# Kernel tuning notes

Hardware: AMD Instinct MI355X
Metric: run time of the kernel (lower is better)

The kernel has to match this reference:

```python
import jax, jax.numpy as jnp
import numpy as np


def setup_inputs() -> dict:
    key = jax.random.key(0)
    k1, k2, k3, k4, k5 = jax.random.split(key, 5)
    B, D, U = 16384, 512, 512
    scale = 1.0 / np.sqrt(D + U)
    return {
        "inputs": jax.random.normal(k1, (B, D), dtype=jnp.float32),
        "h_prev": jax.random.normal(k2, (B, U), dtype=jnp.float32),
        "Wz": jax.random.normal(k3, (D + U, U), dtype=jnp.float32) * scale,
        "Wr": jax.random.normal(k4, (D + U, U), dtype=jnp.float32) * scale,
        "Wh": jax.random.normal(k5, (D + U, U), dtype=jnp.float32) * scale,
    }


def reference(inputs, h_prev, Wz, Wr, Wh):
    # x_h: [B, D+U]
    x_h = jnp.concatenate([inputs, h_prev], axis=-1)
    z = jax.nn.sigmoid(x_h @ Wz)                     # update gate [B, U]
    r = jax.nn.sigmoid(x_h @ Wr)                     # reset gate  [B, U]
    h_hat = jnp.tanh(jnp.concatenate([inputs, r * h_prev], axis=-1) @ Wh)
    new_h = z * h_prev + (1.0 - z) * h_hat
    return new_h
```

## Files before the change

kernel.cpp:

```cpp
#include <hip/hip_runtime.h>
#include <hip/hip_bf16.h>
#include <stdint.h>

typedef __attribute__((ext_vector_type(8))) short short8;
typedef __attribute__((ext_vector_type(4))) float f32x4;
typedef unsigned short u16;

#define AS1 __attribute__((address_space(1)))
#define AS3 __attribute__((address_space(3)))

__device__ __forceinline__ u16 f2b(float f) {
  union { float f; uint32_t u; } c; c.f = f;
  uint32_t u = c.u;
  return (u16)((u + 0x7fffu + ((u >> 16) & 1u)) >> 16);
}
__device__ __forceinline__ float b2f(u16 b) {
  union { uint32_t u; float f; } c; c.u = ((uint32_t)b) << 16;
  return c.f;
}

__global__ void cvt_bf16_kernel(const float* __restrict__ src,
                                u16* __restrict__ dst, int n4) {
  int i = blockIdx.x * blockDim.x + threadIdx.x;
  if (i >= n4) return;
  const float4 v = reinterpret_cast<const float4*>(src)[i];
  ushort4 o;
  o.x = f2b(v.x); o.y = f2b(v.y); o.z = f2b(v.z); o.w = f2b(v.w);
  reinterpret_cast<ushort4*>(dst)[i] = o;
}

__global__ void cvt_transpose_kernel(const float* __restrict__ w0,
                                     const float* __restrict__ w1,
                                     const float* __restrict__ w2,
                                     u16* __restrict__ d0,
                                     u16* __restrict__ d1,
                                     u16* __restrict__ d2,
                                     int K, int N) {
  const float* src = (blockIdx.y == 0) ? w0 : (blockIdx.y == 1 ? w1 : w2);
  u16* dst = (blockIdx.y == 0) ? d0 : (blockIdx.y == 1 ? d1 : d2);
  int idx = blockIdx.x * blockDim.x + threadIdx.x;
  if (idx >= K * N) return;
  int k = idx / N, n = idx - k * N;
  dst[(size_t)n * K + k] = f2b(src[idx]);
}

#define BAR() __builtin_amdgcn_s_barrier()
#define VMW(n) asm volatile("s_waitcnt vmcnt(" #n ")" ::: "memory")

__global__ __launch_bounds__(512, 1) void gemm_gates_kernel(
    const u16* __restrict__ xb, const u16* __restrict__ hb,
    const u16* __restrict__ wt,
    u16* __restrict__ o_z, u16* __restrict__ o_rh) {
  constexpr int NT = 16, NITER = 8;
  __shared__ u16 lds[65536];
  const char* ldsb = (const char*)lds;

  const int tid = threadIdx.x;
  const int lane = tid & 63;
  const int wid = tid >> 6;
  const int wm = wid >> 2, wn = wid & 3;
  const int wg = ((int)blockIdx.x & 7) * 32 + ((int)blockIdx.x >> 3);
  const int bn = wg & 3, bm = wg >> 2;

  const int srow8 = tid >> 3;
  const int swzb = ((tid & 7) ^ (srow8 & 7)) << 4;
  auto STAGE = [&](int t, int kind) {
    if (t >= NT) return;
    u16* dst = lds + (t & 1) * 32768 + kind * 8192 + wid * 512;
    if (kind < 2) {
      const char* src = ((t < 8) ? ((const char*)xb + (size_t)t * 128)
                                 : ((const char*)hb + (size_t)(t - 8) * 128)) +
                        (size_t)(bm * 256 + kind * 128 + srow8) * 1024 + swzb;
      __builtin_amdgcn_global_load_lds((const AS1 void*)src, (AS3 void*)dst, 16, 0, 0);
      __builtin_amdgcn_global_load_lds((const AS1 void*)(src + 65536), (AS3 void*)(dst + 4096), 16, 0, 0);
    } else {
      const char* src = (const char*)wt +
                        (size_t)(bn * 256 + (kind - 2) * 128 + srow8) * 2048 +
                        (size_t)t * 128 + swzb;
      __builtin_amdgcn_global_load_lds((const AS1 void*)src, (AS3 void*)dst, 16, 0, 0);
      __builtin_amdgcn_global_load_lds((const AS1 void*)(src + 131072), (AS3 void*)(dst + 4096), 16, 0, 0);
    }
  };

  const int rsel = lane & 15;
  const int kg = lane >> 4;
  const int sl0 = (kg ^ (rsel & 7)) << 4;
  const int sl1 = ((4 + kg) ^ (rsel & 7)) << 4;
  const int aoff0 = wm * 16384 + rsel * 128;
  const int boff0 = 32768 + wn * 8192 + rsel * 128;

  f32x4 acc[8][4] = {};
  short8 a[4][2], b[4][2];

  auto ldA = [&](int DB, int mfb) {
#pragma unroll
    for (int mi = 0; mi < 4; ++mi) {
      a[mi][0] = *(const short8*)(ldsb + DB + aoff0 + (mfb + mi) * 2048 + sl0);
      a[mi][1] = *(const short8*)(ldsb + DB + aoff0 + (mfb + mi) * 2048 + sl1);
    }
  };
  auto ldB = [&](int DB, int nfb) {
#pragma unroll
    for (int ni = 0; ni < 2; ++ni) {
      b[nfb + ni][0] = *(const short8*)(ldsb + DB + boff0 + (nfb + ni) * 2048 + sl0);
      b[nfb + ni][1] = *(const short8*)(ldsb + DB + boff0 + (nfb + ni) * 2048 + sl1);
    }
  };
  auto MM = [&](int mb, int nb) {
    __builtin_amdgcn_s_setprio(1);
#pragma unroll
    for (int ks = 0; ks < 2; ++ks)
#pragma unroll
      for (int mi = 0; mi < 4; ++mi)
#pragma unroll
        for (int ni = 0; ni < 2; ++ni)
          acc[mb + mi][nb + ni] = __builtin_amdgcn_mfma_f32_16x16x32_bf16(
              a[mi][ks], b[nb + ni][ks], acc[mb + mi][nb + ni], 0, 0, 0);
    __builtin_amdgcn_s_setprio(0);
  };

  STAGE(0, 2); STAGE(0, 3); STAGE(0, 0); STAGE(0, 1); STAGE(1, 2); STAGE(1, 3);
  VMW(4); BAR();

#pragma unroll 1
  for (int j = 0; j < NITER; ++j) {
    const int t1 = 2 * j + 1, t2 = 2 * j + 2, t3 = 2 * j + 3;
    ldA(0, 0); ldB(0, 0); STAGE(t1, 0);
    BAR(); MM(0, 0); BAR();
    ldB(0, 2); STAGE(t1, 1);
    BAR(); MM(0, 2); BAR();
    ldA(0, 4); STAGE(t2, 2);
    BAR(); MM(4, 2); BAR();
    STAGE(t2, 3);
    BAR(); MM(4, 0);
    if (j == NITER - 1) { VMW(0); } else { VMW(4); }
    BAR();
    ldA(65536, 0); ldB(65536, 0); STAGE(t2, 0);
    BAR(); MM(0, 0); BAR();
    ldB(65536, 2); STAGE(t2, 1);
    BAR(); MM(0, 2); BAR();
    ldA(65536, 4); STAGE(t3, 2);
    BAR(); MM(4, 2); BAR();
    STAGE(t3, 3);
    BAR(); MM(4, 0);
    if (j == NITER - 1) { VMW(0); } else { VMW(4); }
    BAR();
  }

  const int row0 = bm * 256 + wm * 128 + kg * 4;
  const int col0 = bn * 256 + wn * 64 + rsel;
  if (bn < 2) {
#pragma unroll
    for (int mf = 0; mf < 8; ++mf)
#pragma unroll
      for (int nf = 0; nf < 4; ++nf)
#pragma unroll
        for (int q = 0; q < 4; ++q) {
          const int row = row0 + mf * 16 + q;
          const int col = col0 + nf * 16;
          const float zf = 1.f / (1.f + __expf(-acc[mf][nf][q]));
          o_z[(size_t)row * 512 + col] = f2b(zf);
        }
  } else {
#pragma unroll
    for (int mf = 0; mf < 8; ++mf)
#pragma unroll
      for (int nf = 0; nf < 4; ++nf)
#pragma unroll
        for (int q = 0; q < 4; ++q) {
          const int row = row0 + mf * 16 + q;
          const int col = col0 + nf * 16 - 512;
          const size_t idx = (size_t)row * 512 + col;
          const float rf = 1.f / (1.f + __expf(-acc[mf][nf][q]));
          o_rh[idx] = f2b(rf * b2f(hb[idx]));
        }
  }
}

__global__ __launch_bounds__(512, 1) void gemm_cand_kernel(
    const u16* __restrict__ xb, const u16* __restrict__ rhb,
    const u16* __restrict__ wt, const u16* __restrict__ hb,
    const u16* __restrict__ zb_in, float* __restrict__ o_f) {
  constexpr int NT = 16;
  __shared__ u16 lds[73728];
  const char* ldsb = (const char*)lds;

  const int tid = threadIdx.x;
  const int lane = tid & 63;
  const int wid = tid >> 6;
  const int wm = wid >> 2, wn = wid & 3;
  const int wg = ((int)blockIdx.x & 7) * 32 + ((int)blockIdx.x >> 3);
  const int bn = wg & 3, bm = wg >> 2;

  const int srow8 = tid >> 3;
  const int swzb = ((tid & 7) ^ (srow8 & 7)) << 4;
  auto STG_A = [&](int t, int half, int regionByte) {
    if (t >= NT) return;
    u16* dst = lds + regionByte / 2 + half * 8192 + wid * 512;
    const char* src = ((t < 8) ? ((const char*)xb + (size_t)t * 128)
                               : ((const char*)rhb + (size_t)(t - 8) * 128)) +
                      (size_t)(bm * 256 + half * 128 + srow8) * 1024 + swzb;
    __builtin_amdgcn_global_load_lds((const AS1 void*)src, (AS3 void*)dst, 16, 0, 0);
    __builtin_amdgcn_global_load_lds((const AS1 void*)(src + 65536), (AS3 void*)(dst + 4096), 16, 0, 0);
  };
  auto STG_B = [&](int t, int regionByte) {
    if (t >= NT) return;
    u16* dst = lds + regionByte / 2 + wid * 512;
    const char* src = (const char*)wt + (size_t)(bn * 128 + srow8) * 2048 +
                      (size_t)t * 128 + swzb;
    __builtin_amdgcn_global_load_lds((const AS1 void*)src, (AS3 void*)dst, 16, 0, 0);
    __builtin_amdgcn_global_load_lds((const AS1 void*)(src + 131072), (AS3 void*)(dst + 4096), 16, 0, 0);
  };

  const int rsel = lane & 15;
  const int kg = lane >> 4;
  const int sl0 = (kg ^ (rsel & 7)) << 4;
  const int sl1 = ((4 + kg) ^ (rsel & 7)) << 4;
  const int aoff0 = wm * 16384 + rsel * 128;
  const int boff0 = wn * 4096 + rsel * 128;

  f32x4 acc[8][2] = {};
  short8 a[4][2], b[2][2];

  auto RD_A = [&](int regionByte, int mfb) {
#pragma unroll
    for (int mi = 0; mi < 4; ++mi) {
      a[mi][0] = *(const short8*)(ldsb + regionByte + aoff0 + (mfb + mi) * 2048 + sl0);
      a[mi][1] = *(const short8*)(ldsb + regionByte + aoff0 + (mfb + mi) * 2048 + sl1);
    }
  };
  auto RD_B = [&](int regionByte) {
#pragma unroll
    for (int ni = 0; ni < 2; ++ni) {
      b[ni][0] = *(const short8*)(ldsb + regionByte + boff0 + ni * 2048 + sl0);
      b[ni][1] = *(const short8*)(ldsb + regionByte + boff0 + ni * 2048 + sl1);
    }
  };
  auto MM = [&](int mb) {
    __builtin_amdgcn_s_setprio(1);
#pragma unroll
    for (int ks = 0; ks < 2; ++ks)
#pragma unroll
      for (int mi = 0; mi < 4; ++mi)
#pragma unroll
        for (int ni = 0; ni < 2; ++ni)
          acc[mb + mi][ni] = __builtin_amdgcn_mfma_f32_16x16x32_bf16(
              a[mi][ks], b[ni][ks], acc[mb + mi][ni], 0, 0, 0);
    __builtin_amdgcn_s_setprio(0);
  };

  STG_B(0, 32768); STG_A(0, 0, 0); STG_A(0, 1, 0);
  STG_A(1, 0, 49152); STG_A(1, 1, 49152); STG_B(1, 114688);
  VMW(6); BAR();

  auto ITER = [&](int j, int pr, bool last) {
    const int e2 = 2 * j + 2, o2 = 2 * j + 3;
    const int OA = 49152 + pr * 32768, OAs = 49152 + (1 - pr) * 32768;
    const int OB = 114688 + pr * 16384, OBs = 114688 + (1 - pr) * 16384;
    RD_A(0, 0); RD_B(32768); STG_A(o2, 0, OAs);
    BAR(); MM(0); BAR();
    RD_A(0, 4); STG_A(o2, 1, OAs); STG_B(e2, 32768);
    BAR(); MM(4);
    if (last) { VMW(0); } else { VMW(6); }
    BAR();
    RD_A(OA, 0); RD_B(OB); STG_A(e2, 0, 0); STG_A(e2, 1, 0); STG_B(o2, OBs);
    BAR(); MM(0); BAR();
    RD_A(OA, 4);
    BAR(); MM(4);
    if (last) { VMW(0); } else { VMW(2); }
    BAR();
  };

#pragma unroll 1
  for (int jj = 0; jj < 4; ++jj) {
    ITER(2 * jj, 0, false);
    ITER(2 * jj + 1, 1, jj == 3);
  }

  const int row0 = bm * 256 + wm * 128 + kg * 4;
  const int col0 = bn * 128 + wn * 32 + rsel;
#pragma unroll
  for (int mf = 0; mf < 8; ++mf)
#pragma unroll
    for (int nf = 0; nf < 2; ++nf)
#pragma unroll
      for (int q = 0; q < 4; ++q) {
        const int row = row0 + mf * 16 + q;
        const int col = col0 + nf * 16;
        const size_t idx = (size_t)row * 512 + col;
        const float s = acc[mf][nf][q];
        const float hh = 2.f / (1.f + __expf(-2.f * s)) - 1.f;
        const float z = b2f(zb_in[idx]);
        o_f[idx] = z * b2f(hb[idx]) + (1.f - z) * hh;
      }
}

extern "C" void kernel_launch(void* const* d_in, const int* in_sizes, int n_in,
                              void* d_out, int out_size, void* d_ws, size_t ws_size,
                              hipStream_t stream) {
  const float* inputs = (const float*)d_in[0];
  const float* h_prev = (const float*)d_in[1];
  const float* Wz = (const float*)d_in[2];
  const float* Wr = (const float*)d_in[3];
  const float* Wh = (const float*)d_in[4];
  float* out = (float*)d_out;

  const int B = 16384, D = 512, U = 512, K = 1024;

  u16* xb = (u16*)d_ws;
  u16* hb = xb + (size_t)B * D;
  u16* wzt = hb + (size_t)B * U;
  u16* wrt = wzt + (size_t)K * U;
  u16* wht = wrt + (size_t)K * U;
  u16* zb = wht + (size_t)K * U;
  u16* rhb = zb + (size_t)B * U;

  const int n4 = (B * D) / 4;
  cvt_bf16_kernel<<<(n4 + 255) / 256, 256, 0, stream>>>(inputs, xb, n4);
  cvt_bf16_kernel<<<(n4 + 255) / 256, 256, 0, stream>>>(h_prev, hb, n4);
  dim3 tg((K * U + 255) / 256, 3);
  cvt_transpose_kernel<<<tg, 256, 0, stream>>>(Wz, Wr, Wh, wzt, wrt, wht, K, U);

  gemm_gates_kernel<<<dim3(256), 512, 0, stream>>>(xb, hb, wzt, zb, rhb);
  gemm_cand_kernel<<<dim3(256), 512, 0, stream>>>(xb, rhb, wht, hb, zb, out);
}
```

Before: 101.7 us.

## Restructure GEMM pipelines to 4-stage K=32 ring with register double-buffering

Both GEMM kernels now use K tiles of 32 instead of 64, with a 4-deep LDS ring buffer and a new swizzle. LDS fragment reads for the next step are issued ahead into alternate register sets (aL0/aL1, b0/b1) and gated by explicit lgkmcnt waits and sched_barriers. The aim is to overlap LDS reads and global-to-LDS loads with MFMA work and to cut the number of barriers per unit of compute. In exchange there are twice as many pipeline steps and more register pressure, and the hand-tuned wait counts are fragile.

Measured after the change: 131.8 us. 1.3x slower.

```diff
diff --git a/kernel.cpp b/kernel.cpp
--- a/kernel.cpp
+++ b/kernel.cpp
@@ -44,106 +44,111 @@
   dst[(size_t)n * K + k] = f2b(src[idx]);
 }
 
+
 #define BAR() __builtin_amdgcn_s_barrier()
-#define VMW(n) asm volatile("s_waitcnt vmcnt(" #n ")" ::: "memory")
-
-__global__ __launch_bounds__(512, 1) void gemm_gates_kernel(
+#define SB() __builtin_amdgcn_sched_barrier(0)
+#define LG(n) do { asm volatile("s_waitcnt lgkmcnt(" #n ")" ::: "memory"); __builtin_amdgcn_sched_barrier(0); } while (0)
+#define VMW(n) do { asm volatile("s_waitcnt vmcnt(" #n ")" ::: "memory"); __builtin_amdgcn_sched_barrier(0); } while (0)
+
+__global__ __launch_bounds__(512, 1) void gates_k(
     const u16* __restrict__ xb, const u16* __restrict__ hb,
     const u16* __restrict__ wt,
     u16* __restrict__ o_z, u16* __restrict__ o_rh) {
-  constexpr int NT = 16, NITER = 8;
+  constexpr int NT = 32;
   __shared__ u16 lds[65536];
   const char* ldsb = (const char*)lds;
 
-  const int tid = threadIdx.x;
-  const int lane = tid & 63;
-  const int wid = tid >> 6;
+  const int tid = threadIdx.x, lane = tid & 63, wid = tid >> 6;
   const int wm = wid >> 2, wn = wid & 3;
   const int wg = ((int)blockIdx.x & 7) * 32 + ((int)blockIdx.x >> 3);
   const int bn = wg & 3, bm = wg >> 2;
 
-  const int srow8 = tid >> 3;
-  const int swzb = ((tid & 7) ^ (srow8 & 7)) << 4;
-  auto STAGE = [&](int t, int kind) {
+  const int srow = tid >> 2;
+  const int scol = ((tid & 3) ^ ((tid >> 3) & 3)) << 4;
+
+  auto STG_A = [&](int t) {
     if (t >= NT) return;
-    u16* dst = lds + (t & 1) * 32768 + kind * 8192 + wid * 512;
-    if (kind < 2) {
-      const char* src = ((t < 8) ? ((const char*)xb + (size_t)t * 128)
-                                 : ((const char*)hb + (size_t)(t - 8) * 128)) +
-                        (size_t)(bm * 256 + kind * 128 + srow8) * 1024 + swzb;
-      __builtin_amdgcn_global_load_lds((const AS1 void*)src, (AS3 void*)dst, 16, 0, 0);
-      __builtin_amdgcn_global_load_lds((const AS1 void*)(src + 65536), (AS3 void*)(dst + 4096), 16, 0, 0);
+    char* dst = (char*)lds + (t & 3) * 32768 + wid * 1024;
+    const char* base = (t < 16) ? ((const char*)xb + (size_t)t * 64)
+                                : ((const char*)hb + (size_t)(t - 16) * 64);
+#pragma unroll
+    for (int i = 0; i < 2; ++i) {
+      const char* src = base + (size_t)(bm * 256 + i * 128 + srow) * 1024 + scol;
+      __builtin_amdgcn_global_load_lds((const AS1 void*)src,
+                                       (AS3 void*)(dst + i * 8192), 16, 0, 0);
+    }
+  };
+  auto STG_B = [&](int t) {
+    if (t >= NT) return;
+    char* dst = (char*)lds + (t & 3) * 32768 + 16384 + wid * 1024;
+#pragma unroll
+    for (int i = 0; i < 2; ++i) {
+      const char* src = (const char*)wt +
+                        (size_t)(bn * 256 + i * 128 + srow) * 2048 +
+                        (size_t)t * 64 + scol;
+      __builtin_amdgcn_global_load_lds((const AS1 void*)src,
+                                       (AS3 void*)(dst + i * 8192), 16, 0, 0);
+    }
+  };
+
+  const int rsel = lane & 15, kg = lane >> 4;
+  const int rcol = (kg ^ ((rsel >> 1) & 3)) << 4;
+  const int aoff = (wm * 128 + rsel) * 64 + rcol;
+  const int boff = 16384 + (wn * 64 + rsel) * 64 + rcol;
+
+  f32x4 acc[8][4] = {};
+  short8 aL0[4], aL1[4], aH[4], b0[4], b1[4];
+
+  auto RD_ALO = [&](auto& d, int t) {
+    const char* p = ldsb + (t & 3) * 32768;
+#pragma unroll
+    for (int i = 0; i < 4; ++i) d[i] = *(const short8*)(p + aoff + i * 1024);
+  };
+  auto RD_AHI = [&](int t) {
+    const char* p = ldsb + (t & 3) * 32768;
+#pragma unroll
+    for (int i = 0; i < 4; ++i) aH[i] = *(const short8*)(p + aoff + (4 + i) * 1024);
+  };
+  auto RD_B = [&](auto& d, int t) {
+    const char* p = ldsb + (t & 3) * 32768;
+#pragma unroll
+    for (int i = 0; i < 4; ++i) d[i] = *(const short8*)(p + boff + i * 1024);
+  };
+  auto MM = [&](auto& A, auto& Bv, int mb) {
+    __builtin_amdgcn_s_setprio(1);
+#pragma unroll
+    for (int mi = 0; mi < 4; ++mi)
+#pragma unroll
+      for (int ni = 0; ni < 4; ++ni)
+        acc[mb + mi][ni] = __builtin_amdgcn_mfma_f32_16x16x32_bf16(
+            A[mi], Bv[ni], acc[mb + mi][ni], 0, 0, 0);
+    __builtin_amdgcn_s_setprio(0);
+  };
+
+  STG_A(0); STG_B(0); STG_A(1); STG_B(1); STG_A(2); STG_B(2);
+  VMW(4); BAR();
+  RD_ALO(aL0, 0); RD_B(b0, 0); SB();
+
+#pragma unroll 1
+  for (int j = 0; j < NT / 2; ++j) {
+    const int te = 2 * j, to = 2 * j + 1;
+    RD_AHI(te); STG_A(te + 3);
+    LG(4); MM(aL0, b0, 0);
+    if (te < 29) { VMW(6); } else { VMW(0); }
+    BAR();
+    RD_ALO(aL1, to); RD_B(b1, to); STG_B(te + 3);
+    LG(8); MM(aH, b0, 4);
+    BAR();
+    RD_AHI(to); STG_A(to + 3);
+    LG(4); MM(aL1, b1, 0);
+    if (to < 29) { VMW(6); } else { VMW(0); }
+    BAR();
+    if (j < NT / 2 - 1) {
+      RD_ALO(aL0, to + 1); RD_B(b0, to + 1); STG_B(to + 3);
+      LG(8); MM(aH, b1, 4);
     } else {
-      const char* src = (const char*)wt +
-                        (size_t)(bn * 256 + (kind - 2) * 128 + srow8) * 2048 +
-                        (size_t)t * 128 + swzb;
-      __builtin_amdgcn_global_load_lds((const AS1 void*)src, (AS3 void*)dst, 16, 0, 0);
-      __builtin_amdgcn_global_load_lds((const AS1 void*)(src + 131072), (AS3 void*)(dst + 4096), 16, 0, 0);
-    }
-  };
-
-  const int rsel = lane & 15;
-  const int kg = lane >> 4;
-  const int sl0 = (kg ^ (rsel & 7)) << 4;
-  const int sl1 = ((4 + kg) ^ (rsel & 7)) << 4;
-  const int aoff0 = wm * 16384 + rsel * 128;
-  const int boff0 = 32768 + wn * 8192 + rsel * 128;
-
-  f32x4 acc[8][4] = {};
-  short8 a[4][2], b[4][2];
-
-  auto ldA = [&](int DB, int mfb) {
-#pragma unroll
-    for (int mi = 0; mi < 4; ++mi) {
-      a[mi][0] = *(const short8*)(ldsb + DB + aoff0 + (mfb + mi) * 2048 + sl0);
-      a[mi][1] = *(const short8*)(ldsb + DB + aoff0 + (mfb + mi) * 2048 + sl1);
-    }
-  };
-  auto ldB = [&](int DB, int nfb) {
-#pragma unroll
-    for (int ni = 0; ni < 2; ++ni) {
-      b[nfb + ni][0] = *(const short8*)(ldsb + DB + boff0 + (nfb + ni) * 2048 + sl0);
-      b[nfb + ni][1] = *(const short8*)(ldsb + DB + boff0 + (nfb + ni) * 2048 + sl1);
-    }
-  };
-  auto MM = [&](int mb, int nb) {
-    __builtin_amdgcn_s_setprio(1);
-#pragma unroll
-    for (int ks = 0; ks < 2; ++ks)
-#pragma unroll
-      for (int mi = 0; mi < 4; ++mi)
-#pragma unroll
-        for (int ni = 0; ni < 2; ++ni)
-          acc[mb + mi][nb + ni] = __builtin_amdgcn_mfma_f32_16x16x32_bf16(
-              a[mi][ks], b[nb + ni][ks], acc[mb + mi][nb + ni], 0, 0, 0);
-    __builtin_amdgcn_s_setprio(0);
-  };
-
-  STAGE(0, 2); STAGE(0, 3); STAGE(0, 0); STAGE(0, 1); STAGE(1, 2); STAGE(1, 3);
-  VMW(4); BAR();
-
-#pragma unroll 1
-  for (int j = 0; j < NITER; ++j) {
-    const int t1 = 2 * j + 1, t2 = 2 * j + 2, t3 = 2 * j + 3;
-    ldA(0, 0); ldB(0, 0); STAGE(t1, 0);
-    BAR(); MM(0, 0); BAR();
-    ldB(0, 2); STAGE(t1, 1);
-    BAR(); MM(0, 2); BAR();
-    ldA(0, 4); STAGE(t2, 2);
-    BAR(); MM(4, 2); BAR();
-    STAGE(t2, 3);
-    BAR(); MM(4, 0);
-    if (j == NITER - 1) { VMW(0); } else { VMW(4); }
-    BAR();
-    ldA(65536, 0); ldB(65536, 0); STAGE(t2, 0);
-    BAR(); MM(0, 0); BAR();
-    ldB(65536, 2); STAGE(t2, 1);
-    BAR(); MM(0, 2); BAR();
-    ldA(65536, 4); STAGE(t3, 2);
-    BAR(); MM(4, 2); BAR();
-    STAGE(t3, 3);
-    BAR(); MM(4, 0);
-    if (j == NITER - 1) { VMW(0); } else { VMW(4); }
+      LG(0); MM(aH, b1, 4);
+    }
     BAR();
   }
 
@@ -177,104 +182,101 @@
   }
 }
 
-__global__ __launch_bounds__(512, 1) void gemm_cand_kernel(
+__global__ __launch_bounds__(512, 1) void cand_k(
     const u16* __restrict__ xb, const u16* __restrict__ rhb,
     const u16* __restrict__ wt, const u16* __restrict__ hb,
     const u16* __restrict__ zb_in, float* __restrict__ o_f) {
-  constexpr int NT = 16;
-  __shared__ u16 lds[73728];
+  constexpr int NT = 32;
+  __shared__ u16 lds[49152];
   const char* ldsb = (const char*)lds;
 
-  const int tid = threadIdx.x;
-  const int lane = tid & 63;
-  const int wid = tid >> 6;
+  const int tid = threadIdx.x, lane = tid & 63, wid = tid >> 6;
   const int wm = wid >> 2, wn = wid & 3;
   const int wg = ((int)blockIdx.x & 7) * 32 + ((int)blockIdx.x >> 3);
   const int bn = wg & 3, bm = wg >> 2;
 
-  const int srow8 = tid >> 3;
-  const int swzb = ((tid & 7) ^ (srow8 & 7)) << 4;
-  auto STG_A = [&](int t, int half, int regionByte) {
+  const int srow = tid >> 2;
+  const int scol = ((tid & 3) ^ ((tid >> 3) & 3)) << 4;
+
+  auto STG_A = [&](int t) {
     if (t >= NT) return;
-    u16* dst = lds + regionByte / 2 + half * 8192 + wid * 512;
-    const char* src = ((t < 8) ? ((const char*)xb + (size_t)t * 128)
-                               : ((const char*)rhb + (size_t)(t - 8) * 128)) +
-                      (size_t)(bm * 256 + half * 128 + srow8) * 1024 + swzb;
+    char* dst = (char*)lds + (t & 3) * 24576 + wid * 1024;
+    const char* base = (t < 16) ? ((const char*)xb + (size_t)t * 64)
+                                : ((const char*)rhb + (size_t)(t - 16) * 64);
+#pragma unroll
+    for (int i = 0; i < 2; ++i) {
+      const char* src = base + (size_t)(bm * 256 + i * 128 + srow) * 1024 + scol;
+      __builtin_amdgcn_global_load_lds((const AS1 void*)src,
+                                       (AS3 void*)(dst + i * 8192), 16, 0, 0);
+    }
+  };
+  auto STG_B = [&](int t) {
+    if (t >= NT) return;
+    char* dst = (char*)lds + (t & 3) * 24576 + 16384 + wid * 1024;
+    const char* src = (const char*)wt +
+                      (size_t)(bn * 128 + srow) * 2048 + (size_t)t * 64 + scol;
     __builtin_amdgcn_global_load_lds((const AS1 void*)src, (AS3 void*)dst, 16, 0, 0);
-    __builtin_amdgcn_global_load_lds((const AS1 void*)(src + 65536), (AS3 void*)(dst + 4096), 16, 0, 0);
-  };
-  auto STG_B = [&](int t, int regionByte) {
-    if (t >= NT) return;
-    u16* dst = lds + regionByte / 2 + wid * 512;
-    const char* src = (const char*)wt + (size_t)(bn * 128 + srow8) * 2048 +
-                      (size_t)t * 128 + swzb;
-    __builtin_amdgcn_global_load_lds((const AS1 void*)src, (AS3 void*)dst, 16, 0, 0);
-    __builtin_amdgcn_global_load_lds((const AS1 void*)(src + 131072), (AS3 void*)(dst + 4096), 16, 0, 0);
-  };
-
-  const int rsel = lane & 15;
-  const int kg = lane >> 4;
-  const int sl0 = (kg ^ (rsel & 7)) << 4;
-  const int sl1 = ((4 + kg) ^ (rsel & 7)) << 4;
-  const int aoff0 = wm * 16384 + rsel * 128;
-  const int boff0 = wn * 4096 + rsel * 128;
+  };
+
+  const int rsel = lane & 15, kg = lane >> 4;
+  const int rcol = (kg ^ ((rsel >> 1) & 3)) << 4;
+  const int aoff = (wm * 128 + rsel) * 64 + rcol;
+  const int boff = 16384 + (wn * 32 + rsel) * 64 + rcol;
 
   f32x4 acc[8][2] = {};
-  short8 a[4][2], b[2][2];
-
-  auto RD_A = [&](int regionByte, int mfb) {
-#pragma unroll
-    for (int mi = 0; mi < 4; ++mi) {
-      a[mi][0] = *(const short8*)(ldsb + regionByte + aoff0 + (mfb + mi) * 2048 + sl0);
-      a[mi][1] = *(const short8*)(ldsb + regionByte + aoff0 + (mfb + mi) * 2048 + sl1);
-    }
-  };
-  auto RD_B = [&](int regionByte) {
-#pragma unroll
-    for (int ni = 0; ni < 2; ++ni) {
-      b[ni][0] = *(const short8*)(ldsb + regionByte + boff0 + ni * 2048 + sl0);
-      b[ni][1] = *(const short8*)(ldsb + regionByte + boff0 + ni * 2048 + sl1);
-    }
-  };
-  auto MM = [&](int mb) {
+  short8 aL0[4], aL1[4], aH[4], b0[2], b1[2];
+
+  auto RD_ALO = [&](auto& d, int t) {
+    const char* p = ldsb + (t & 3) * 24576;
+#pragma unroll
+    for (int i = 0; i < 4; ++i) d[i] = *(const short8*)(p + aoff + i * 1024);
+  };
+  auto RD_AHI = [&](int t) {
+    const char* p = ldsb + (t & 3) * 24576;
+#pragma unroll
+    for (int i = 0; i < 4; ++i) aH[i] = *(const short8*)(p + aoff + (4 + i) * 1024);
+  };
+  auto RD_B = [&](auto& d, int t) {
+    const char* p = ldsb + (t & 3) * 24576;
+#pragma unroll
+    for (int i = 0; i < 2; ++i) d[i] = *(const short8*)(p + boff + i * 1024);
+  };
+  auto MM = [&](auto& A, auto& Bv, int mb) {
     __builtin_amdgcn_s_setprio(1);
 #pragma unroll
-    for (int ks = 0; ks < 2; ++ks)
-#pragma unroll
-      for (int mi = 0; mi < 4; ++mi)
-#pragma unroll
-        for (int ni = 0; ni < 2; ++ni)
-          acc[mb + mi][ni] = __builtin_amdgcn_mfma_f32_16x16x32_bf16(
-              a[mi][ks], b[ni][ks], acc[mb + mi][ni], 0, 0, 0);
+    for (int mi = 0; mi < 4; ++mi)
+#pragma unroll
+      for (int ni = 0; ni < 2; ++ni)
+        acc[mb + mi][ni] = __builtin_amdgcn_mfma_f32_16x16x32_bf16(
+            A[mi], Bv[ni], acc[mb + mi][ni], 0, 0, 0);
     __builtin_amdgcn_s_setprio(0);
   };
 
-  STG_B(0, 32768); STG_A(0, 0, 0); STG_A(0, 1, 0);
-  STG_A(1, 0, 49152); STG_A(1, 1, 49152); STG_B(1, 114688);
-  VMW(6); BAR();
-
-  auto ITER = [&](int j, int pr, bool last) {
-    const int e2 = 2 * j + 2, o2 = 2 * j + 3;
-    const int OA = 49152 + pr * 32768, OAs = 49152 + (1 - pr) * 32768;
-    const int OB = 114688 + pr * 16384, OBs = 114688 + (1 - pr) * 16384;
-    RD_A(0, 0); RD_B(32768); STG_A(o2, 0, OAs);
-    BAR(); MM(0); BAR();
-    RD_A(0, 4); STG_A(o2, 1, OAs); STG_B(e2, 32768);
-    BAR(); MM(4);
-    if (last) { VMW(0); } else { VMW(6); }
-    BAR();
-    RD_A(OA, 0); RD_B(OB); STG_A(e2, 0, 0); STG_A(e2, 1, 0); STG_B(o2, OBs);
-    BAR(); MM(0); BAR();
-    RD_A(OA, 4);
-    BAR(); MM(4);
-    if (last) { VMW(0); } else { VMW(2); }
-    BAR();
-  };
+  STG_A(0); STG_B(0); STG_A(1); STG_B(1); STG_A(2); STG_B(2);
+  VMW(3); BAR();
+  RD_ALO(aL0, 0); RD_B(b0, 0); SB();
 
 #pragma unroll 1
-  for (int jj = 0; jj < 4; ++jj) {
-    ITER(2 * jj, 0, false);
-    ITER(2 * jj + 1, 1, jj == 3);
+  for (int j = 0; j < NT / 2; ++j) {
+    const int te = 2 * j, to = 2 * j + 1;
+    RD_AHI(te); STG_A(te + 3);
+    LG(4); MM(aL0, b0, 0);
+    if (te < 29) { VMW(5); } else { VMW(0); }
+    BAR();
+    RD_ALO(aL1, to); RD_B(b1, to); STG_B(te + 3);
+    LG(6); MM(aH, b0, 4);
+    BAR();
+    RD_AHI(to); STG_A(to + 3);
+    LG(4); MM(aL1, b1, 0);
+    if (to < 29) { VMW(5); } else { VMW(0); }
+    BAR();
+    if (j < NT / 2 - 1) {
+      RD_ALO(aL0, to + 1); RD_B(b0, to + 1); STG_B(to + 3);
+      LG(6); MM(aH, b1, 4);
+    } else {
+      LG(0); MM(aH, b1, 4);
+    }
+    BAR();
   }
 
   const int row0 = bm * 256 + wm * 128 + kg * 4;
@@ -321,6 +323,6 @@
   dim3 tg((K * U + 255) / 256, 3);
   cvt_transpose_kernel<<<tg, 256, 0, stream>>>(Wz, Wr, Wh, wzt, wrt, wht, K, U);
 
-  gemm_gates_kernel<<<dim3(256), 512, 0, stream>>>(xb, hb, wzt, zb, rhb);
-  gemm_cand_kernel<<<dim3(256), 512, 0, stream>>>(xb, rhb, wht, hb, zb, out);
-}
+  gates_k<<<dim3(256), 512, 0, stream>>>(xb, hb, wzt, zb, rhb);
+  cand_k<<<dim3(256), 512, 0, stream>>>(xb, rhb, wht, hb, zb, out);
+}
```
